# Performance work log

Hardware: AMD Instinct MI355X
Metric: run time of the kernel (lower is better)

## Reference

```python
import jax, jax.numpy as jnp
import numpy as np

QMIN, QMAX = -128, 127  # 8-bit signed quantized range


def setup_inputs() -> dict:
    key = jax.random.key(0)
    k0, k1, k2, k3 = jax.random.split(key, 4)
    N, Cin, H, W = 64, 128, 56, 56
    Cout, K = 128, 3
    x = jax.random.randint(k0, (N, Cin, H, W), -128, 128, dtype=jnp.int32).astype(jnp.int8)
    weight = jax.random.randint(k1, (Cout, Cin, K, K), -128, 128, dtype=jnp.int32).astype(jnp.int8)
    # int32 bias (already shifted by -Zx*sum(W) in the original quantization flow)
    bias = jax.random.randint(k2, (Cout,), -4096, 4096, dtype=jnp.int32)
    input_scale = jnp.float32(0.02)
    weight_scale = jax.random.uniform(k3, (Cout,), minval=0.001, maxval=0.01, dtype=jnp.float32)  # per-channel
    output_scale = jnp.float32(0.05)
    input_zero_point = -3   # python int, constant
    output_zero_point = -2  # python int, constant
    return {"x": x, "weight": weight, "bias": bias,
            "input_scale": input_scale, "weight_scale": weight_scale,
            "output_scale": output_scale,
            "input_zero_point": input_zero_point,
            "output_zero_point": output_zero_point}


def reference(x, weight, bias, input_scale, weight_scale, output_scale,
              input_zero_point, output_zero_point):
    # pad spatial dims with the INPUT zero point (padding=(1,1), as in the torch module)
    xp = jnp.pad(x, ((0, 0), (0, 0), (1, 1), (1, 1)), constant_values=input_zero_point)
    acc = jax.lax.conv_general_dilated(
        xp.astype(jnp.int32), weight.astype(jnp.int32),
        window_strides=(1, 1), padding='VALID',
        rhs_dilation=(1, 1), dimension_numbers=('NCHW', 'OIHW', 'NCHW'))
    acc = acc + bias[None, :, None, None]                       # [N,Co,Ho,Wo] int32
    # requantize: per-output-channel scale, shift by output zero point
    scale = (input_scale * weight_scale / output_scale)[None, :, None, None]
    out = acc.astype(jnp.float32) * scale + jnp.float32(output_zero_point)
    return jnp.clip(jnp.round(out), QMIN, QMAX).astype(jnp.int8)
```

## Files before the change

### kernel.cpp

```cpp
#include <hip/hip_runtime.h>


#define CIN  128
#define COUT 128
#define HW   56
#define NPIX (HW * HW)
#define ROWS  4
#define QCOLS 58
#define XROW  (QCOLS * CIN)
#define XP_OFF 147456
#define XP_ROWS (64 * QCOLS)

typedef int v4i  __attribute__((ext_vector_type(4)));
typedef int v16i __attribute__((ext_vector_type(16)));

__device__ __forceinline__ void gl16(const void* g, void* l) {
    __builtin_amdgcn_global_load_lds(
        (const __attribute__((address_space(1))) unsigned*)g,
        (__attribute__((address_space(3))) unsigned*)l, 16, 0, 0);
}

__global__ __launch_bounds__(256) void pack_w2(const int* __restrict__ w_g,
                                               unsigned* __restrict__ wp2) {
    int i = blockIdx.x * 256 + threadIdx.x;
    if (i >= 36 * 128 * 8) return;
    int dw   = i & 7;
    int cout = (i >> 3) & 127;
    int step = i >> 10;
    int t  = step >> 2;
    int cb = step & 3;
    unsigned d = 0;
#pragma unroll
    for (int b = 0; b < 4; ++b) {
        int ci = cb * 32 + dw * 4 + b;
        int v = w_g[(cout * CIN + ci) * 9 + t];
        d |= (unsigned)(v & 0xFF) << (8 * b);
    }
    int g  = (cout << 1) | (dw >> 2);
    int gs = g ^ ((g >> 3) & 7);
    wp2[step * 1024 + gs * 4 + (dw & 3)] = d;
}

#define LSTR 57
__global__ __launch_bounds__(256) void repack_x(const int* __restrict__ x_g,
                                                unsigned char* __restrict__ xp,
                                                const int* __restrict__ zp_in_p) {
    __shared__ int lx[CIN * LSTR];
    const int blk = blockIdx.x;
    const int n  = blk / QCOLS;
    const int hp = blk % QCOLS;
    const int tid = threadIdx.x;
    const unsigned zpd = (unsigned)((*zp_in_p) & 0xFF) * 0x01010101u;
    unsigned* row = (unsigned*)(xp + (size_t)blk * XROW);

    if (hp == 0 || hp == QCOLS - 1) {
#pragma unroll
        for (int it = 0; it < 8; ++it) {
            int d = it * 256 + tid;
            if (d < QCOLS * 32) row[d] = zpd;
        }
        return;
    }
    const int h = hp - 1;
    const int* xrow = x_g + (n * CIN * HW + h) * HW;
#pragma unroll
    for (int it = 0; it < 7; ++it) {
        int idx = it * 256 + tid;
        int ci  = idx / 14;
        int w4  = (idx - ci * 14) * 4;
        v4i L = *(const v4i*)(xrow + ci * NPIX + w4);
        int* ld = &lx[ci * LSTR + w4];
        ld[0] = L[0]; ld[1] = L[1]; ld[2] = L[2]; ld[3] = L[3];
    }
    __syncthreads();
#pragma unroll
    for (int it = 0; it < 8; ++it) {
        int d = it * 256 + tid;
        if (d < QCOLS * 32) {
            int wp  = d >> 5;
            int ci4 = d & 31;
            unsigned v = zpd;
            if (wp >= 1 && wp <= HW) {
                const int* lb = &lx[ci4 * 4 * LSTR + (wp - 1)];
                v = (unsigned)(lb[0] & 0xFF) |
                    ((unsigned)(lb[LSTR] & 0xFF) << 8) |
                    ((unsigned)(lb[2 * LSTR] & 0xFF) << 16) |
                    ((unsigned)(lb[3 * LSTR] & 0xFF) << 24);
            }
            row[d] = v;
        }
    }
}

__global__ __launch_bounds__(256, 2) void conv_mfma(
    const unsigned char* __restrict__ xp, const unsigned char* __restrict__ wp2b,
    const int* __restrict__ bias, const float* __restrict__ in_s,
    const float* __restrict__ w_s, const float* __restrict__ out_s,
    const int* __restrict__ zp_out_p, int* __restrict__ out) {
    __shared__ unsigned char xsb[45056];
    __shared__ unsigned char Bb2[2][8192];
    __shared__ float scs[COUT];
    __shared__ int   bis[COUT];

    const int n   = blockIdx.x / 14;
    const int ho0 = (blockIdx.x % 14) * ROWS;
    const int tid    = threadIdx.x;
    const int lane   = tid & 63;
    const int wave   = tid >> 6;
    const int lane31 = lane & 31;
    const int hi     = lane >> 5;
    const int hi4    = hi * 4;

    if (tid < COUT) {
        scs[tid] = ((*in_s) / (*out_s)) * w_s[tid];
        bis[tid] = bias[tid];
    }

    const unsigned char* win = xp + (size_t)(n * QCOLS + ho0) * XROW;
    const int qrel = lane >> 3;
    const int lof  = (qrel * 8 + ((lane & 7) ^ qrel)) * 16;
    for (int i = wave; i < 44; i += 4) {
        int off = i * 1024 + lof;
        if (i == 43 && qrel >= 4) off = lof & 0;
        gl16(win + off, xsb + i * 1024);
    }
    {
        const unsigned char* bs = wp2b + wave * 2048 + lane * 16;
        gl16(bs, &Bb2[0][wave * 2048]);
        gl16(bs + 1024, &Bb2[0][wave * 2048 + 1024]);
    }
    __syncthreads();

    const unsigned* xs = (const unsigned*)xsb;
    int qb[2];
#pragma unroll
    for (int i = 0; i < 2; ++i) {
        int px = (wave * 2 + i) * 32 + lane31;
        if (px > ROWS * HW - 1) px = ROWS * HW - 1;
        qb[i] = (px / HW) * QCOLS + (px % HW);
    }
    int boff[4];
#pragma unroll
    for (int nt = 0; nt < 4; ++nt) {
        int g = nt * 64 + lane31 * 2 + hi;
        boff[nt] = (g ^ ((g >> 3) & 7)) * 16;
    }

    v16i acc[2][4];
#pragma unroll
    for (int i = 0; i < 2; ++i)
#pragma unroll
        for (int j = 0; j < 4; ++j) acc[i][j] = (v16i)0;

#pragma unroll 1
    for (int u = 0; u < 18; ++u) {
        if (u < 17) {
            const unsigned char* bs = wp2b + (u + 1) * 8192 + wave * 2048 + lane * 16;
            unsigned char* bd = &Bb2[(u + 1) & 1][wave * 2048];
            gl16(bs, bd);
            gl16(bs + 1024, bd + 1024);
        }
        const int t  = u >> 1;
        const int dq = (t / 3) * QCOLS + (t % 3);
        const int q0 = qb[0] + dq, q1 = qb[1] + dq;
        const int s0 = (q0 & 7) << 2, s1 = (q1 & 7) << 2;
        const unsigned char* bb = Bb2[u & 1];
#pragma unroll
        for (int c = 0; c < 2; ++c) {
            const int cb = (u & 1) * 2 + c;
            v4i a0 = *(const v4i*)&xs[q0 * 32 + ((cb * 8 + hi4) ^ s0)];
            v4i a1 = *(const v4i*)&xs[q1 * 32 + ((cb * 8 + hi4) ^ s1)];
            const unsigned char* bc = bb + c * 4096;
            v4i b0 = *(const v4i*)(bc + boff[0]);
            v4i b1 = *(const v4i*)(bc + boff[1]);
            v4i b2 = *(const v4i*)(bc + boff[2]);
            v4i b3 = *(const v4i*)(bc + boff[3]);
            acc[0][0] = __builtin_amdgcn_mfma_i32_32x32x32_i8(b0, a0, acc[0][0], 0, 0, 0);
            acc[0][1] = __builtin_amdgcn_mfma_i32_32x32x32_i8(b1, a0, acc[0][1], 0, 0, 0);
            acc[0][2] = __builtin_amdgcn_mfma_i32_32x32x32_i8(b2, a0, acc[0][2], 0, 0, 0);
            acc[0][3] = __builtin_amdgcn_mfma_i32_32x32x32_i8(b3, a0, acc[0][3], 0, 0, 0);
            acc[1][0] = __builtin_amdgcn_mfma_i32_32x32x32_i8(b0, a1, acc[1][0], 0, 0, 0);
            acc[1][1] = __builtin_amdgcn_mfma_i32_32x32x32_i8(b1, a1, acc[1][1], 0, 0, 0);
            acc[1][2] = __builtin_amdgcn_mfma_i32_32x32x32_i8(b2, a1, acc[1][2], 0, 0, 0);
            acc[1][3] = __builtin_amdgcn_mfma_i32_32x32x32_i8(b3, a1, acc[1][3], 0, 0, 0);
        }
        __syncthreads();
    }

    const float zpo = (float)(*zp_out_p);
#pragma unroll
    for (int i = 0; i < 2; ++i) {
        const int px = (wave * 2 + i) * 32 + lane31;
        if (px < ROWS * HW) {
            int* ob = out + n * COUT * NPIX + ho0 * HW + px;
#pragma unroll
            for (int nt = 0; nt < 4; ++nt) {
#pragma unroll
                for (int reg = 0; reg < 16; ++reg) {
                    int co = nt * 32 + (reg & 3) + 8 * (reg >> 2) + hi4;
                    float f = fmaf((float)(acc[i][nt][reg] + bis[co]), scs[co], zpo);
                    f = rintf(f);
                    f = fminf(fmaxf(f, -128.0f), 127.0f);
                    ob[co * NPIX] = (int)f;
                }
            }
        }
    }
}

extern "C" void kernel_launch(void* const* d_in, const int* in_sizes, int n_in,
                              void* d_out, int out_size, void* d_ws, size_t ws_size,
                              hipStream_t stream) {
    const int* x_g      = (const int*)d_in[0];
    const int* w_g      = (const int*)d_in[1];
    const int* bias     = (const int*)d_in[2];
    const float* in_s   = (const float*)d_in[3];
    const float* w_s    = (const float*)d_in[4];
    const float* out_s  = (const float*)d_in[5];
    const int* zp_in_p  = (const int*)d_in[6];
    const int* zp_out_p = (const int*)d_in[7];
    int* outp = (int*)d_out;
    unsigned* wp2 = (unsigned*)d_ws;
    unsigned char* xpp = (unsigned char*)d_ws + XP_OFF;

    pack_w2<<<(36 * 128 * 8 + 255) / 256, 256, 0, stream>>>(w_g, wp2);
    repack_x<<<XP_ROWS, 256, 0, stream>>>(x_g, xpp, zp_in_p);

    const int nblocks = 64 * (HW / ROWS);
    conv_mfma<<<nblocks, 256, 0, stream>>>(xpp, (const unsigned char*)wp2, bias,
                                           in_s, w_s, out_s, zp_out_p, outp);
}
```

Measured before the change: 85.81 us.

## Load weight fragments directly from global into registers with triple buffering

Weight tiles no longer go through a double-buffered LDS stage. Each lane now loads its MFMA B fragments straight from global (L2-resident packed weights) into a three-deep register rotation, prefetching two steps ahead. This removes the LDS staging and the per-step __syncthreads barrier from the main loop, so waves can run independently. In exchange every wave issues redundant global loads for the same weights and needs more VGPRs, which may limit occupancy or expose global latency.

Measured after the change: 86.74 us. About the same (+1.1%).

```diff
diff --git a/kernel.cpp b/kernel.cpp
--- a/kernel.cpp
+++ b/kernel.cpp
@@ -10,6 +10,7 @@
 #define XROW  (QCOLS * CIN)
 #define XP_OFF 147456
 #define XP_ROWS (64 * QCOLS)
+#define STEPS 36
 
 typedef int v4i  __attribute__((ext_vector_type(4)));
 typedef int v16i __attribute__((ext_vector_type(16)));
@@ -98,7 +99,6 @@
     const float* __restrict__ w_s, const float* __restrict__ out_s,
     const int* __restrict__ zp_out_p, int* __restrict__ out) {
     __shared__ unsigned char xsb[45056];
-    __shared__ unsigned char Bb2[2][8192];
     __shared__ float scs[COUT];
     __shared__ int   bis[COUT];
 
@@ -121,76 +121,81 @@
     const int lof  = (qrel * 8 + ((lane & 7) ^ qrel)) * 16;
     for (int i = wave; i < 44; i += 4) {
         int off = i * 1024 + lof;
-        if (i == 43 && qrel >= 4) off = lof & 0;
+        if (i == 43 && qrel >= 4) off = 0;
         gl16(win + off, xsb + i * 1024);
     }
+    __syncthreads();
+
+    const unsigned* xs = (const unsigned*)xsb;
+    int qb0, qb1;
     {
-        const unsigned char* bs = wp2b + wave * 2048 + lane * 16;
-        gl16(bs, &Bb2[0][wave * 2048]);
-        gl16(bs + 1024, &Bb2[0][wave * 2048 + 1024]);
-    }
-    __syncthreads();
-
-    const unsigned* xs = (const unsigned*)xsb;
-    int qb[2];
+        int px0 = wave * 64 + lane31;
+        int px1 = wave * 64 + 32 + lane31;
+        if (px1 > ROWS * HW - 1) px1 = ROWS * HW - 1;
+        qb0 = (px0 / HW) * QCOLS + (px0 % HW);
+        qb1 = (px1 / HW) * QCOLS + (px1 % HW);
+    }
+    const unsigned char *bpA, *bpB, *bpC, *bpD;
+    {
+        int g0 = 0 * 64 + lane31 * 2 + hi;
+        int g1 = 1 * 64 + lane31 * 2 + hi;
+        int g2 = 2 * 64 + lane31 * 2 + hi;
+        int g3 = 3 * 64 + lane31 * 2 + hi;
+        bpA = wp2b + (g0 ^ ((g0 >> 3) & 7)) * 16;
+        bpB = wp2b + (g1 ^ ((g1 >> 3) & 7)) * 16;
+        bpC = wp2b + (g2 ^ ((g2 >> 3) & 7)) * 16;
+        bpD = wp2b + (g3 ^ ((g3 >> 3) & 7)) * 16;
+    }
+
+    v16i acc[2][4];
+#pragma unroll
+    for (int i = 0; i < 2; ++i)
+#pragma unroll
+        for (int j = 0; j < 4; ++j) acc[i][j] = (v16i)0;
+
+    v4i c0[4], c1[4], c2[4];
+#define LOADB(DST, S)                                                        \
+    {                                                                        \
+        DST[0] = *(const v4i*)(bpA + (S) * 4096);                            \
+        DST[1] = *(const v4i*)(bpB + (S) * 4096);                            \
+        DST[2] = *(const v4i*)(bpC + (S) * 4096);                            \
+        DST[3] = *(const v4i*)(bpD + (S) * 4096);                            \
+    }
+#define BODY(S, CUR, NX2)                                                    \
+    {                                                                        \
+        if ((S) + 2 < STEPS) LOADB(NX2, (S) + 2);                            \
+        const int t2 = (S) >> 2, cb = (S) & 3;                               \
+        const int kr = (t2 * 11) >> 5;                                       \
+        const int dq = kr * QCOLS + (t2 - 3 * kr);                           \
+        const int q0 = qb0 + dq, q1 = qb1 + dq;                              \
+        v4i a0 = *(const v4i*)&xs[q0 * 32 + ((cb * 8 + hi4) ^ ((q0 & 7) << 2))]; \
+        v4i a1 = *(const v4i*)&xs[q1 * 32 + ((cb * 8 + hi4) ^ ((q1 & 7) << 2))]; \
+        acc[0][0] = __builtin_amdgcn_mfma_i32_32x32x32_i8(CUR[0], a0, acc[0][0], 0, 0, 0); \
+        acc[0][1] = __builtin_amdgcn_mfma_i32_32x32x32_i8(CUR[1], a0, acc[0][1], 0, 0, 0); \
+        acc[0][2] = __builtin_amdgcn_mfma_i32_32x32x32_i8(CUR[2], a0, acc[0][2], 0, 0, 0); \
+        acc[0][3] = __builtin_amdgcn_mfma_i32_32x32x32_i8(CUR[3], a0, acc[0][3], 0, 0, 0); \
+        acc[1][0] = __builtin_amdgcn_mfma_i32_32x32x32_i8(CUR[0], a1, acc[1][0], 0, 0, 0); \
+        acc[1][1] = __builtin_amdgcn_mfma_i32_32x32x32_i8(CUR[1], a1, acc[1][1], 0, 0, 0); \
+        acc[1][2] = __builtin_amdgcn_mfma_i32_32x32x32_i8(CUR[2], a1, acc[1][2], 0, 0, 0); \
+        acc[1][3] = __builtin_amdgcn_mfma_i32_32x32x32_i8(CUR[3], a1, acc[1][3], 0, 0, 0); \
+    }
+
+    LOADB(c0, 0);
+    LOADB(c1, 1);
+#pragma unroll 1
+    for (int uu = 0; uu < 12; ++uu) {
+        const int s = uu * 3;
+        BODY(s + 0, c0, c2);
+        BODY(s + 1, c1, c0);
+        BODY(s + 2, c2, c1);
+    }
+#undef BODY
+#undef LOADB
+
+    const float zpo = (float)(*zp_out_p);
 #pragma unroll
     for (int i = 0; i < 2; ++i) {
-        int px = (wave * 2 + i) * 32 + lane31;
-        if (px > ROWS * HW - 1) px = ROWS * HW - 1;
-        qb[i] = (px / HW) * QCOLS + (px % HW);
-    }
-    int boff[4];
-#pragma unroll
-    for (int nt = 0; nt < 4; ++nt) {
-        int g = nt * 64 + lane31 * 2 + hi;
-        boff[nt] = (g ^ ((g >> 3) & 7)) * 16;
-    }
-
-    v16i acc[2][4];
-#pragma unroll
-    for (int i = 0; i < 2; ++i)
-#pragma unroll
-        for (int j = 0; j < 4; ++j) acc[i][j] = (v16i)0;
-
-#pragma unroll 1
-    for (int u = 0; u < 18; ++u) {
-        if (u < 17) {
-            const unsigned char* bs = wp2b + (u + 1) * 8192 + wave * 2048 + lane * 16;
-            unsigned char* bd = &Bb2[(u + 1) & 1][wave * 2048];
-            gl16(bs, bd);
-            gl16(bs + 1024, bd + 1024);
-        }
-        const int t  = u >> 1;
-        const int dq = (t / 3) * QCOLS + (t % 3);
-        const int q0 = qb[0] + dq, q1 = qb[1] + dq;
-        const int s0 = (q0 & 7) << 2, s1 = (q1 & 7) << 2;
-        const unsigned char* bb = Bb2[u & 1];
-#pragma unroll
-        for (int c = 0; c < 2; ++c) {
-            const int cb = (u & 1) * 2 + c;
-            v4i a0 = *(const v4i*)&xs[q0 * 32 + ((cb * 8 + hi4) ^ s0)];
-            v4i a1 = *(const v4i*)&xs[q1 * 32 + ((cb * 8 + hi4) ^ s1)];
-            const unsigned char* bc = bb + c * 4096;
-            v4i b0 = *(const v4i*)(bc + boff[0]);
-            v4i b1 = *(const v4i*)(bc + boff[1]);
-            v4i b2 = *(const v4i*)(bc + boff[2]);
-            v4i b3 = *(const v4i*)(bc + boff[3]);
-            acc[0][0] = __builtin_amdgcn_mfma_i32_32x32x32_i8(b0, a0, acc[0][0], 0, 0, 0);
-            acc[0][1] = __builtin_amdgcn_mfma_i32_32x32x32_i8(b1, a0, acc[0][1], 0, 0, 0);
-            acc[0][2] = __builtin_amdgcn_mfma_i32_32x32x32_i8(b2, a0, acc[0][2], 0, 0, 0);
-            acc[0][3] = __builtin_amdgcn_mfma_i32_32x32x32_i8(b3, a0, acc[0][3], 0, 0, 0);
-            acc[1][0] = __builtin_amdgcn_mfma_i32_32x32x32_i8(b0, a1, acc[1][0], 0, 0, 0);
-            acc[1][1] = __builtin_amdgcn_mfma_i32_32x32x32_i8(b1, a1, acc[1][1], 0, 0, 0);
-            acc[1][2] = __builtin_amdgcn_mfma_i32_32x32x32_i8(b2, a1, acc[1][2], 0, 0, 0);
-            acc[1][3] = __builtin_amdgcn_mfma_i32_32x32x32_i8(b3, a1, acc[1][3], 0, 0, 0);
-        }
-        __syncthreads();
-    }
-
-    const float zpo = (float)(*zp_out_p);
-#pragma unroll
-    for (int i = 0; i < 2; ++i) {
-        const int px = (wave * 2 + i) * 32 + lane31;
+        const int px = wave * 64 + i * 32 + lane31;
         if (px < ROWS * HW) {
             int* ob = out + n * COUT * NPIX + ho0 * HW + px;
 #pragma unroll
```
